# Kernel tuning notes

Hardware: AMD Instinct MI355X
Metric: run time of the kernel (lower is better)

Reference implementation:

```python
import jax, jax.numpy as jnp
import numpy as np

N_NODES = 50000
N_EDGES = 600000
IN_DIM = 128
OUT_DIM = 128
NEG_SLOPE = 0.2
LN_EPS = 1e-5


def setup_inputs() -> dict:
    key = jax.random.key(0)
    ks = jax.random.split(key, 8)
    x = jax.random.normal(ks[0], (N_NODES, IN_DIM), dtype=jnp.float32)
    edge_index = jax.random.randint(ks[1], (2, N_EDGES), 0, N_NODES, dtype=jnp.int64)
    glorot = float(np.sqrt(6.0 / (IN_DIM + OUT_DIM)))
    W_l = jax.random.uniform(ks[2], (IN_DIM, OUT_DIM), jnp.float32, -glorot, glorot)
    W_r = jax.random.uniform(ks[3], (IN_DIM, OUT_DIM), jnp.float32, -glorot, glorot)
    att = jax.random.uniform(ks[4], (OUT_DIM,), jnp.float32, -glorot, glorot)
    bias = jnp.zeros((OUT_DIM,), jnp.float32)
    ln_gamma = jnp.ones((OUT_DIM,), jnp.float32)
    ln_beta = jnp.zeros((OUT_DIM,), jnp.float32)
    return {"x": x, "edge_index": edge_index, "W_l": W_l, "W_r": W_r,
            "att": att, "bias": bias, "ln_gamma": ln_gamma, "ln_beta": ln_beta}


def _gatv2_ln(x, edge_index, W_l, W_r, att, bias, ln_gamma, ln_beta):
    N = x.shape[0]
    # add self loops (PyG GATv2Conv default add_self_loops=True)
    loop = jnp.arange(N, dtype=edge_index.dtype)
    src = jnp.concatenate([edge_index[0], loop])  # [E+N]
    dst = jnp.concatenate([edge_index[1], loop])
    x_l = x @ W_l  # [N, D] transformed source features
    x_r = x @ W_r  # [N, D] transformed target features
    # GATv2 edge score: e_ij = a^T LeakyReLU(x_l[src] + x_r[dst])
    h = jax.nn.leaky_relu(x_l[src] + x_r[dst], NEG_SLOPE)  # [E+N, D]
    e = h @ att  # [E+N]
    # segment softmax over incoming edges of each dst node
    m = jax.lax.stop_gradient(jax.ops.segment_max(e, dst, num_segments=N))
    ex = jnp.exp(e - m[dst])
    denom = jax.ops.segment_sum(ex, dst, num_segments=N)
    alpha = ex / denom[dst]  # [E+N] (denom > 0 thanks to self loops)
    # weighted scatter-add aggregation (dropout=0.1 is inference no-op)
    out = jax.ops.segment_sum(alpha[:, None] * x_l[src], dst, num_segments=N)
    out = out + bias  # heads=1, concat=False -> mean over 1 head = identity
    # LayerNorm over feature dim
    mu = jnp.mean(out, axis=-1, keepdims=True)
    var = jnp.var(out, axis=-1, keepdims=True)
    return (out - mu) * jax.lax.rsqrt(var + LN_EPS) * ln_gamma + ln_beta


def reference(x, edge_index, W_l, W_r, att, bias, ln_gamma, ln_beta):
    return _gatv2_ln(x, edge_index, W_l, W_r, att, bias, ln_gamma, ln_beta)
```

## Files before the change

kernel.cpp:

```cpp
#include <hip/hip_runtime.h>
#include <hip/hip_bf16.h>


constexpr int NN  = 50000;
constexpr int NE  = 600000;
constexpr int D   = 128;
constexpr int CAP = 64;
constexpr int MT  = 80;
constexpr int GEMM_THREADS = 320;

typedef __attribute__((ext_vector_type(8))) short bf16x8;
typedef __attribute__((ext_vector_type(4))) float f32x4;

__device__ __forceinline__ ushort f2bf(float f) {
  uint u = __builtin_bit_cast(uint, f);
  return (ushort)((u + 0x7FFFu + ((u >> 16) & 1u)) >> 16);
}
__device__ __forceinline__ float bflo(uint u) { return __builtin_bit_cast(float, u << 16); }
__device__ __forceinline__ float bfhi(uint u) { return __builtin_bit_cast(float, u & 0xFFFF0000u); }
__device__ __forceinline__ void unpack8(uint4 u, float* v) {
  v[0] = bflo(u.x); v[1] = bfhi(u.x);
  v[2] = bflo(u.y); v[3] = bfhi(u.y);
  v[4] = bflo(u.z); v[5] = bfhi(u.z);
  v[6] = bflo(u.w); v[7] = bfhi(u.w);
}

__global__ __launch_bounds__(256) void k_wpack(const float* __restrict__ Wl,
    const float* __restrict__ Wr, ushort* __restrict__ wpk) {
  const int t = blockIdx.x * 256 + threadIdx.x;
  if (t >= 2 * 4 * 8 * 64) return;
  const int lane = t & 63;
  const int ct   = (t >> 6) & 7;
  const int ks   = (t >> 9) & 3;
  const int wh   = t >> 11;
  const float* W = wh ? Wr : Wl;
  const int c  = ct * 16 + (lane & 15);
  const int k0 = ks * 32 + (lane >> 4) * 8;
  ushort v[8];
#pragma unroll
  for (int j = 0; j < 8; ++j) v[j] = f2bf(W[(k0 + j) * D + c]);
  *(bf16x8*)&wpk[(size_t)t * 8] = *(bf16x8*)v;
}

__global__ __launch_bounds__(GEMM_THREADS) void k_gemm(const float* __restrict__ x,
    const ushort* __restrict__ wpk, ushort* __restrict__ xl,
    ushort* __restrict__ xr) {
  __shared__ __align__(16) ushort axs[MT * D];
  const int t = threadIdx.x;
  const int row0 = blockIdx.x * MT;
  for (int ch = t; ch < MT * 16; ch += GEMM_THREADS) {
    const int r = ch >> 4, kc = ch & 15;
    const float4* src = (const float4*)&x[(size_t)(row0 + r) * D + kc * 8];
    const float4 f0 = src[0], f1 = src[1];
    ushort pk[8];
    pk[0] = f2bf(f0.x); pk[1] = f2bf(f0.y); pk[2] = f2bf(f0.z); pk[3] = f2bf(f0.w);
    pk[4] = f2bf(f1.x); pk[5] = f2bf(f1.y); pk[6] = f2bf(f1.z); pk[7] = f2bf(f1.w);
    uint byte = (uint)(r * 256 + kc * 16);
    byte ^= (uint)((r & 7) << 4);
    *(bf16x8*)((char*)axs + byte) = *(bf16x8*)pk;
  }
  __syncthreads();
  const int w = t >> 6, l = t & 63;
  f32x4 accl[8], accr[8];
#pragma unroll
  for (int ct = 0; ct < 8; ++ct) { accl[ct] = (f32x4)0.f; accr[ct] = (f32x4)0.f; }
  const bf16x8* wv = (const bf16x8*)wpk;
  const int rloc = w * 16 + (l & 15);
#pragma unroll
  for (int ks = 0; ks < 4; ++ks) {
    uint byte = (uint)(rloc * 256 + ks * 64 + ((l >> 4) << 4));
    byte ^= (uint)((rloc & 7) << 4);
    const bf16x8 a = *(const bf16x8*)((const char*)axs + byte);
#pragma unroll
    for (int ct = 0; ct < 8; ++ct) {
      const bf16x8 bl = wv[((0 * 4 + ks) * 8 + ct) * 64 + l];
      const bf16x8 br = wv[((1 * 4 + ks) * 8 + ct) * 64 + l];
      accl[ct] = __builtin_amdgcn_mfma_f32_16x16x32_bf16(a, bl, accl[ct], 0, 0, 0);
      accr[ct] = __builtin_amdgcn_mfma_f32_16x16x32_bf16(a, br, accr[ct], 0, 0, 0);
    }
  }
  const int rl0 = w * 16 + ((l >> 4) << 2);
  const int cl  = l & 15;
#pragma unroll
  for (int ct = 0; ct < 8; ++ct) {
    const int col = ct * 16 + cl;
#pragma unroll
    for (int i = 0; i < 4; ++i) {
      const size_t o = (size_t)(row0 + rl0 + i) * D + col;
      xl[o] = f2bf(accl[ct][i]);
      xr[o] = f2bf(accr[ct][i]);
    }
  }
}

__global__ __launch_bounds__(256) void k_init(int* __restrict__ cnt,
                                              int* __restrict__ eidx) {
  const int n = blockIdx.x * 256 + threadIdx.x;
  if (n < NN) { cnt[n] = 1; eidx[n * CAP] = n; }
}

__global__ __launch_bounds__(256) void k_fill(const int* __restrict__ ei,
    int* __restrict__ cnt, int* __restrict__ eidx) {
  const int e = blockIdx.x * 256 + threadIdx.x;
  if (e < NE) {
    const int src = ei[e];
    const int dst = ei[NE + e];
    const int pos = atomicAdd(&cnt[dst], 1);
    if (pos < CAP) eidx[dst * CAP + pos] = src;
  }
}

__global__ __launch_bounds__(256) void k_node(const int* __restrict__ cnt,
    const int* __restrict__ eidx,
    const ushort* __restrict__ xl, const ushort* __restrict__ xr,
    const float* __restrict__ att, const float* __restrict__ bias,
    const float* __restrict__ gamma, const float* __restrict__ beta,
    float* __restrict__ out) {
  const int n = blockIdx.x * 4 + (threadIdx.x >> 6);
  const int lane = threadIdx.x & 63;
  const int eg = lane & 3;
  const int ls = lane >> 2;
  const int d0 = ls * 8;
  constexpr float LOG2E = 1.4426950408889634f;

  float vr[8], av[8];
  unpack8(*(const uint4*)&xr[(uint)n * D + d0], vr);
  *(float4*)&av[0] = *(const float4*)&att[d0];
  *(float4*)&av[4] = *(const float4*)&att[d0 + 4];

  const int m    = min(cnt[n], CAP);
  const int base = n * CAP;
  float acc[8] = {0.f,0.f,0.f,0.f,0.f,0.f,0.f,0.f};
  float den = 0.f;

  for (int p0 = 0; p0 < m; p0 += 4) {
    const int pe  = p0 + eg;
    const bool act = (pe < m);
    const int src = act ? eidx[base + pe] : 0;
    float v[8];
    unpack8(*(const uint4*)&xl[(uint)src * D + d0], v);
    float p[8];
#pragma unroll
    for (int j = 0; j < 8; ++j) {
      float h = v[j] + vr[j];
      h = fmaxf(h, 0.2f * h);
      p[j] = h * av[j];
    }
    float s = ((p[0] + p[1]) + (p[2] + p[3])) + ((p[4] + p[5]) + (p[6] + p[7]));
    s += __shfl_xor(s, 4);
    s += __shfl_xor(s, 8);
    s += __shfl_xor(s, 16);
    s += __shfl_xor(s, 32);
    const float e = act ? exp2f(s * LOG2E) : 0.f;
    den += e;
#pragma unroll
    for (int j = 0; j < 8; ++j) acc[j] = fmaf(e, v[j], acc[j]);
  }
#pragma unroll
  for (int j = 0; j < 8; ++j) {
    acc[j] += __shfl_xor(acc[j], 1);
    acc[j] += __shfl_xor(acc[j], 2);
  }
  den += __shfl_xor(den, 1);
  den += __shfl_xor(den, 2);
  const float inv = 1.0f / den;

  float o[8];
  {
    const float4 b0 = *(const float4*)&bias[d0];
    const float4 b1 = *(const float4*)&bias[d0 + 4];
    o[0] = fmaf(acc[0], inv, b0.x); o[1] = fmaf(acc[1], inv, b0.y);
    o[2] = fmaf(acc[2], inv, b0.z); o[3] = fmaf(acc[3], inv, b0.w);
    o[4] = fmaf(acc[4], inv, b1.x); o[5] = fmaf(acc[5], inv, b1.y);
    o[6] = fmaf(acc[6], inv, b1.z); o[7] = fmaf(acc[7], inv, b1.w);
  }
  float sm = 0.f, sq = 0.f;
#pragma unroll
  for (int j = 0; j < 8; ++j) { sm += o[j]; sq = fmaf(o[j], o[j], sq); }
  sm += __shfl_xor(sm, 4);  sq += __shfl_xor(sq, 4);
  sm += __shfl_xor(sm, 8);  sq += __shfl_xor(sq, 8);
  sm += __shfl_xor(sm, 16); sq += __shfl_xor(sq, 16);
  sm += __shfl_xor(sm, 32); sq += __shfl_xor(sq, 32);
  const float mean = sm * (1.0f / D);
  const float var  = sq * (1.0f / D) - mean * mean;
  const float rstd = rsqrtf(var + 1e-5f);
  if (eg == 0) {
    const float4 g0 = *(const float4*)&gamma[d0];
    const float4 g1 = *(const float4*)&gamma[d0 + 4];
    const float4 be0 = *(const float4*)&beta[d0];
    const float4 be1 = *(const float4*)&beta[d0 + 4];
    float4 o0, o1;
    o0.x = (o[0] - mean) * rstd * g0.x + be0.x;
    o0.y = (o[1] - mean) * rstd * g0.y + be0.y;
    o0.z = (o[2] - mean) * rstd * g0.z + be0.z;
    o0.w = (o[3] - mean) * rstd * g0.w + be0.w;
    o1.x = (o[4] - mean) * rstd * g1.x + be1.x;
    o1.y = (o[5] - mean) * rstd * g1.y + be1.y;
    o1.z = (o[6] - mean) * rstd * g1.z + be1.z;
    o1.w = (o[7] - mean) * rstd * g1.w + be1.w;
    *(float4*)&out[(size_t)n * D + d0]     = o0;
    *(float4*)&out[(size_t)n * D + d0 + 4] = o1;
  }
}

extern "C" void kernel_launch(void* const* d_in, const int* in_sizes, int n_in,
                              void* d_out, int out_size, void* d_ws, size_t ws_size,
                              hipStream_t stream) {
  const float* x     = (const float*)d_in[0];
  const int*   ei    = (const int*)d_in[1];
  const float* Wl    = (const float*)d_in[2];
  const float* Wr    = (const float*)d_in[3];
  const float* att   = (const float*)d_in[4];
  const float* bias  = (const float*)d_in[5];
  const float* gamma = (const float*)d_in[6];
  const float* beta  = (const float*)d_in[7];
  float* out = (float*)d_out;

  char* ws = (char*)d_ws;
  ushort* xl   = (ushort*)ws;
  ushort* xr   = xl + (size_t)NN * D;
  int*    eidx = (int*)(xr + (size_t)NN * D);
  int*    cnt  = eidx + (size_t)NN * CAP;
  ushort* wpk  = (ushort*)(cnt + NN);

  k_wpack<<<16, 256, 0, stream>>>(Wl, Wr, wpk);
  k_init<<<(NN + 255) / 256, 256, 0, stream>>>(cnt, eidx);
  k_gemm<<<NN / MT, GEMM_THREADS, 0, stream>>>(x, wpk, xl, xr);
  k_fill<<<(NE + 255) / 256, 256, 0, stream>>>(ei, cnt, eidx);
  k_node<<<NN / 4, 256, 0, stream>>>(cnt, eidx, xl, xr, att, bias, gamma,
                                     beta, out);
}
```

Measured before the change: 187.8 us.

## Handle self-loop in registers, prefetch neighbor rows, replace init kernel with memset

The self-loop edge is no longer stored in the adjacency bucket. Its score and contribution are computed directly from the node's own xl row, which is already loaded, and folded in after the reduction. The neighbor loop now software-pipelines the index and feature loads two iterations ahead, to hide gather latency in the memory-bound aggregation. The k_init kernel is replaced by a hipMemsetAsync on the counts. Together these cut one launch and one dependent load per node, at the cost of more registers and some redundant prefetch loads past the end of each bucket.

```diff
diff --git a/kernel.cpp b/kernel.cpp
--- a/kernel.cpp
+++ b/kernel.cpp
@@ -93,12 +93,6 @@
   }
 }
 
-__global__ __launch_bounds__(256) void k_init(int* __restrict__ cnt,
-                                              int* __restrict__ eidx) {
-  const int n = blockIdx.x * 256 + threadIdx.x;
-  if (n < NN) { cnt[n] = 1; eidx[n * CAP] = n; }
-}
-
 __global__ __launch_bounds__(256) void k_fill(const int* __restrict__ ei,
     int* __restrict__ cnt, int* __restrict__ eidx) {
   const int e = blockIdx.x * 256 + threadIdx.x;
@@ -123,30 +117,56 @@
   const int d0 = ls * 8;
   constexpr float LOG2E = 1.4426950408889634f;
 
-  float vr[8], av[8];
+  float vr[8], av[8], vs[8];
   unpack8(*(const uint4*)&xr[(uint)n * D + d0], vr);
+  unpack8(*(const uint4*)&xl[(uint)n * D + d0], vs);
   *(float4*)&av[0] = *(const float4*)&att[d0];
   *(float4*)&av[4] = *(const float4*)&att[d0 + 4];
 
   const int m    = min(cnt[n], CAP);
   const int base = n * CAP;
+
+  float ss = 0.f;
+#pragma unroll
+  for (int j = 0; j < 8; ++j) {
+    float h = vs[j] + vr[j];
+    h = fmaxf(h, 0.2f * h);
+    ss = fmaf(h, av[j], ss);
+  }
+  ss += __shfl_xor(ss, 4);
+  ss += __shfl_xor(ss, 8);
+  ss += __shfl_xor(ss, 16);
+  ss += __shfl_xor(ss, 32);
+  const float eself = exp2f(ss * LOG2E);
+
   float acc[8] = {0.f,0.f,0.f,0.f,0.f,0.f,0.f,0.f};
   float den = 0.f;
 
+  int s1 = (eg < m) ? eidx[base + eg] : n;
+  uint4 u = *(const uint4*)&xl[(uint)s1 * D + d0];
+  s1 = (4 + eg < m) ? eidx[base + 4 + eg] : n;
+
   for (int p0 = 0; p0 < m; p0 += 4) {
-    const int pe  = p0 + eg;
-    const bool act = (pe < m);
-    const int src = act ? eidx[base + pe] : 0;
+    uint4 un = *(const uint4*)&xl[(uint)s1 * D + d0];
+    const int pe2 = p0 + 8 + eg;
+    const int s2 = (pe2 < m) ? eidx[base + pe2] : n;
+    const bool act = (p0 + eg < m);
     float v[8];
-    unpack8(*(const uint4*)&xl[(uint)src * D + d0], v);
-    float p[8];
-#pragma unroll
-    for (int j = 0; j < 8; ++j) {
-      float h = v[j] + vr[j];
-      h = fmaxf(h, 0.2f * h);
-      p[j] = h * av[j];
-    }
-    float s = ((p[0] + p[1]) + (p[2] + p[3])) + ((p[4] + p[5]) + (p[6] + p[7]));
+    unpack8(u, v);
+    float h0, h1;
+    h0 = v[0] + vr[0]; h0 = fmaxf(h0, 0.2f * h0);
+    h1 = v[1] + vr[1]; h1 = fmaxf(h1, 0.2f * h1);
+    float t0 = fmaf(h0, av[0], h1 * av[1]);
+    h0 = v[2] + vr[2]; h0 = fmaxf(h0, 0.2f * h0);
+    h1 = v[3] + vr[3]; h1 = fmaxf(h1, 0.2f * h1);
+    float t1 = fmaf(h0, av[2], h1 * av[3]);
+    h0 = v[4] + vr[4]; h0 = fmaxf(h0, 0.2f * h0);
+    h1 = v[5] + vr[5]; h1 = fmaxf(h1, 0.2f * h1);
+    float t2 = fmaf(h0, av[4], h1 * av[5]);
+    h0 = v[6] + vr[6]; h0 = fmaxf(h0, 0.2f * h0);
+    h1 = v[7] + vr[7]; h1 = fmaxf(h1, 0.2f * h1);
+    float t3 = fmaf(h0, av[6], h1 * av[7]);
+    float s = (t0 + t1) + (t2 + t3);
     s += __shfl_xor(s, 4);
     s += __shfl_xor(s, 8);
     s += __shfl_xor(s, 16);
@@ -155,6 +175,7 @@
     den += e;
 #pragma unroll
     for (int j = 0; j < 8; ++j) acc[j] = fmaf(e, v[j], acc[j]);
+    u = un; s1 = s2;
   }
 #pragma unroll
   for (int j = 0; j < 8; ++j) {
@@ -163,6 +184,9 @@
   }
   den += __shfl_xor(den, 1);
   den += __shfl_xor(den, 2);
+  den += eself;
+#pragma unroll
+  for (int j = 0; j < 8; ++j) acc[j] = fmaf(eself, vs[j], acc[j]);
   const float inv = 1.0f / den;
 
   float o[8];
@@ -223,8 +247,8 @@
   int*    cnt  = eidx + (size_t)NN * CAP;
   ushort* wpk  = (ushort*)(cnt + NN);
 
+  hipMemsetAsync(cnt, 0, NN * sizeof(int), stream);
   k_wpack<<<16, 256, 0, stream>>>(Wl, Wr, wpk);
-  k_init<<<(NN + 255) / 256, 256, 0, stream>>>(cnt, eidx);
   k_gemm<<<NN / MT, GEMM_THREADS, 0, stream>>>(x, wpk, xl, xr);
   k_fill<<<(NE + 255) / 256, 256, 0, stream>>>(ei, cnt, eidx);
   k_node<<<NN / 4, 256, 0, stream>>>(cnt, eidx, xl, xr, att, bias, gamma,
```

Result: faster. 181.7 us (-3.3%).
